# Kernel tuning notes

Measured on AMD Instinct MI355X. Metric: run time of the kernel, lower is better.

The kernel has to match this reference:

```python
import jax, jax.numpy as jnp
import numpy as np

GAMMA = 1.0
N, M, D = 1024, 128, 128  # M must equal embed_dim D for the original numpy broadcast


def setup_inputs() -> dict:
    key = jax.random.key(0)
    k1, k2, k3, k4 = jax.random.split(key, 4)
    a = jax.random.normal(k1, (N, D), dtype=jnp.float32)
    b = jax.random.normal(k2, (M, D), dtype=jnp.float32)
    rotation_params = jax.random.normal(k3, (D, D), dtype=jnp.float32)
    entangle_params = jax.random.normal(k4, (D, D), dtype=jnp.float32)
    return {"a": a, "b": b, "rotation_params": rotation_params,
            "entangle_params": entangle_params}


def reference(a, b, rotation_params, entangle_params):
    d = a.shape[-1]
    # --- RBF Gram matrix (replaces nested python loops): ||x-y||^2 expansion ---
    sq = (jnp.sum(a * a, axis=1)[:, None]
          + jnp.sum(b * b, axis=1)[None, :]
          - 2.0 * (a @ b.T))                      # [N, M]
    K = jnp.exp(-GAMMA * sq)                       # [N, M]
    # --- batched self-attention, each row of `a` is a length-1 sequence ---
    q = a @ rotation_params.reshape(d, -1)         # [N, d]
    k = a @ entangle_params.reshape(d, -1)         # [N, d]
    logits = jnp.sum(q * k, axis=-1, keepdims=True) / float(np.sqrt(d))  # [N, 1]
    scores = jax.nn.softmax(logits, axis=-1)       # == 1 (single key per query)
    attn_weights = scores * a                      # [N, d] (scores @ value for len-1 seq)
    # --- K * attn_weights[:, None]: numpy broadcast (N,M)*(N,1,d) -> (N,N,d) ---
    # out[i, j, kk] = K[j, kk] * attn_weights[i, kk]
    return K[None, :, :] * attn_weights[:, None, :]  # [N, N, D]
```

## Files before the change

kernel.cpp:

```cpp
#include <hip/hip_runtime.h>
#include <math.h>


#define GAMMA_F 1.0f
#define N_ROWS 1024
#define DIM    128

__global__ __launch_bounds__(DIM) void compute_K_kernel(
    const float* __restrict__ a,
    const float* __restrict__ b,
    float* __restrict__ K)
{
    __shared__ float4 a_sh[DIM / 4];
    const int j = blockIdx.x;
    const int m = threadIdx.x;

    if (m < DIM / 4) {
        a_sh[m] = reinterpret_cast<const float4*>(a + (size_t)j * DIM)[m];
    }
    __syncthreads();

    const float4* b4 = reinterpret_cast<const float4*>(b + (size_t)m * DIM);
    float acc = 0.0f;
#pragma unroll 8
    for (int d = 0; d < DIM / 4; ++d) {
        const float4 av = a_sh[d];
        const float4 bv = b4[d];
        const float dx = av.x - bv.x;
        const float dy = av.y - bv.y;
        const float dz = av.z - bv.z;
        const float dw = av.w - bv.w;
        acc = fmaf(dx, dx, acc);
        acc = fmaf(dy, dy, acc);
        acc = fmaf(dz, dz, acc);
        acc = fmaf(dw, dw, acc);
    }
    K[(size_t)j * DIM + m] = expf(-GAMMA_F * acc);
}

__global__ __launch_bounds__(256) void bcast_mul_kernel(
    const float4* __restrict__ a4,
    const float4* __restrict__ K4,
    float4* __restrict__ out4,
    unsigned n_vec)
{
    const unsigned v = blockIdx.x * 256u + threadIdx.x;
    if (v >= n_vec) return;

    const unsigned k4  = v & 31u;
    const unsigned row = v >> 5;
    const unsigned j   = row & 1023u;
    const unsigned i   = row >> 10;

    const float4 av = a4[i * 32u + k4];
    const float4 kv = K4[j * 32u + k4];

    float4 o;
    o.x = av.x * kv.x;
    o.y = av.y * kv.y;
    o.z = av.z * kv.z;
    o.w = av.w * kv.w;
    out4[v] = o;
}

extern "C" void kernel_launch(void* const* d_in, const int* in_sizes, int n_in,
                              void* d_out, int out_size, void* d_ws, size_t ws_size,
                              hipStream_t stream)
{
    const float* a = reinterpret_cast<const float*>(d_in[0]);
    const float* b = reinterpret_cast<const float*>(d_in[1]);

    float* K = reinterpret_cast<float*>(d_ws);

    compute_K_kernel<<<N_ROWS, DIM, 0, stream>>>(a, b, K);

    const unsigned n_vec = (unsigned)(out_size / 4);
    const unsigned blocks = (n_vec + 255u) / 256u;
    bcast_mul_kernel<<<blocks, 256, 0, stream>>>(
        reinterpret_cast<const float4*>(a),
        reinterpret_cast<const float4*>(K),
        reinterpret_cast<float4*>(d_out),
        n_vec);
}
```

Baseline: 533.2 us.

## Fuse RBF row computation into broadcast-multiply kernel with nontemporal stores

Merges the Gram-row computation and the broadcast multiply into one kernel. Each block recomputes one K row in shared memory and writes a 256-row tile of the output. This removes the second launch and the workspace round trip for K, and uses nontemporal stores and a per-thread loop to stream the large output. In exchange, each K row is recomputed four times and the store addresses per warp become strided across rows.

```diff
diff --git a/kernel.cpp b/kernel.cpp
--- a/kernel.cpp
+++ b/kernel.cpp
@@ -3,64 +3,70 @@
 
 
 #define GAMMA_F 1.0f
-#define N_ROWS 1024
-#define DIM    128
+#define N_ROWS  1024
+#define DIM     128
+#define I_TILE  256
+#define N_ITILE (N_ROWS / I_TILE)
+#define THREADS 256
 
-__global__ __launch_bounds__(DIM) void compute_K_kernel(
+typedef float floatx4 __attribute__((ext_vector_type(4)));
+
+__global__ __launch_bounds__(THREADS) void fused_bcast_kernel(
     const float* __restrict__ a,
     const float* __restrict__ b,
-    float* __restrict__ K)
+    floatx4* __restrict__ out4)
 {
     __shared__ float4 a_sh[DIM / 4];
-    const int j = blockIdx.x;
-    const int m = threadIdx.x;
+    __shared__ float  k_row[DIM];
 
-    if (m < DIM / 4) {
-        a_sh[m] = reinterpret_cast<const float4*>(a + (size_t)j * DIM)[m];
+    const int bid = blockIdx.x;
+    const int j   = bid >> 2;
+    const int i0  = (bid & 3) * I_TILE;
+    const int tid = threadIdx.x;
+
+    if (tid < DIM / 4) {
+        a_sh[tid] = reinterpret_cast<const float4*>(a + (size_t)j * DIM)[tid];
     }
     __syncthreads();
 
-    const float4* b4 = reinterpret_cast<const float4*>(b + (size_t)m * DIM);
-    float acc = 0.0f;
+    if (tid < DIM) {
+        const float4* b4 = reinterpret_cast<const float4*>(b + (size_t)tid * DIM);
+        float acc = 0.0f;
 #pragma unroll 8
-    for (int d = 0; d < DIM / 4; ++d) {
-        const float4 av = a_sh[d];
-        const float4 bv = b4[d];
-        const float dx = av.x - bv.x;
-        const float dy = av.y - bv.y;
-        const float dz = av.z - bv.z;
-        const float dw = av.w - bv.w;
-        acc = fmaf(dx, dx, acc);
-        acc = fmaf(dy, dy, acc);
-        acc = fmaf(dz, dz, acc);
-        acc = fmaf(dw, dw, acc);
+        for (int d = 0; d < DIM / 4; ++d) {
+            const float4 av = a_sh[d];
+            const float4 bv = b4[d];
+            const float dx = av.x - bv.x;
+            const float dy = av.y - bv.y;
+            const float dz = av.z - bv.z;
+            const float dw = av.w - bv.w;
+            acc = fmaf(dx, dx, acc);
+            acc = fmaf(dy, dy, acc);
+            acc = fmaf(dz, dz, acc);
+            acc = fmaf(dw, dw, acc);
+        }
+        k_row[tid] = expf(-GAMMA_F * acc);
     }
-    K[(size_t)j * DIM + m] = expf(-GAMMA_F * acc);
-}
+    __syncthreads();
 
-__global__ __launch_bounds__(256) void bcast_mul_kernel(
-    const float4* __restrict__ a4,
-    const float4* __restrict__ K4,
-    float4* __restrict__ out4,
-    unsigned n_vec)
-{
-    const unsigned v = blockIdx.x * 256u + threadIdx.x;
-    if (v >= n_vec) return;
+    const int k4 = tid & 31;
+    const int ir = tid >> 5;
+    const floatx4 kv = reinterpret_cast<const floatx4*>(k_row)[k4];
 
-    const unsigned k4  = v & 31u;
-    const unsigned row = v >> 5;
-    const unsigned j   = row & 1023u;
-    const unsigned i   = row >> 10;
+    const floatx4* __restrict__ a4 = reinterpret_cast<const floatx4*>(a);
+    const int i_base = i0 + ir;
+    size_t o_idx = ((size_t)i_base * N_ROWS + j) * (DIM / 4) + k4;
+    size_t a_idx = (size_t)i_base * (DIM / 4) + k4;
 
-    const float4 av = a4[i * 32u + k4];
-    const float4 kv = K4[j * 32u + k4];
+    const size_t o_step = (size_t)8 * N_ROWS * (DIM / 4);
+    const size_t a_step = (size_t)8 * (DIM / 4);
 
-    float4 o;
-    o.x = av.x * kv.x;
-    o.y = av.y * kv.y;
-    o.z = av.z * kv.z;
-    o.w = av.w * kv.w;
-    out4[v] = o;
+#pragma unroll 8
+    for (int it = 0; it < I_TILE / 8; ++it) {
+        const floatx4 av = a4[a_idx + (size_t)it * a_step];
+        const floatx4 o  = av * kv;
+        __builtin_nontemporal_store(o, &out4[o_idx + (size_t)it * o_step]);
+    }
 }
 
 extern "C" void kernel_launch(void* const* d_in, const int* in_sizes, int n_in,
@@ -70,15 +76,6 @@
     const float* a = reinterpret_cast<const float*>(d_in[0]);
     const float* b = reinterpret_cast<const float*>(d_in[1]);
 
-    float* K = reinterpret_cast<float*>(d_ws);
-
-    compute_K_kernel<<<N_ROWS, DIM, 0, stream>>>(a, b, K);
-
-    const unsigned n_vec = (unsigned)(out_size / 4);
-    const unsigned blocks = (n_vec + 255u) / 256u;
-    bcast_mul_kernel<<<blocks, 256, 0, stream>>>(
-        reinterpret_cast<const float4*>(a),
-        reinterpret_cast<const float4*>(K),
-        reinterpret_cast<float4*>(d_out),
-        n_vec);
+    fused_bcast_kernel<<<N_ROWS * N_ITILE, THREADS, 0, stream>>>(
+        a, b, reinterpret_cast<floatx4*>(d_out));
 }
```

Result: no change. 539.5 us (+1.2%).
